# Kernel tuning notes

Measured on AMD Instinct MI355X. Metric: run time of the kernel, lower is better.

## Reference

```python
import jax, jax.numpy as jnp
import numpy as np

B, N, E, H = 2, 4096, 1024, 16
HD = E // H                      # head_dim = 64
R = 8                            # LoRA rank
LORA_SCALE = 16.0 / R            # alpha / r = 2.0
BUCKET_SIZES = (256, 64, 16)


def setup_inputs() -> dict:
    key = jax.random.key(0)
    ks = jax.random.split(key, 24)
    inp = {"x": jax.random.normal(ks[0], (B, N, E), jnp.float32)}
    inp["wb_coarse"] = jax.random.randint(ks[1], (B, N), 0, 16)
    inp["wb_mid"] = jax.random.randint(ks[2], (B, N), 0, 64)
    inp["wb_fine"] = jax.random.randint(ks[3], (B, N), 0, 256)
    i = 4
    for name in ("q", "k", "v", "o"):
        inp[f"W{name}"] = jax.random.normal(ks[i], (E, E), jnp.float32) / np.sqrt(E); i += 1
        inp[f"b{name}"] = jax.random.normal(ks[i], (E,), jnp.float32) * 0.01; i += 1
        inp[f"A{name}"] = jax.random.normal(ks[i], (R, E), jnp.float32) / np.sqrt(E); i += 1
        inp[f"B{name}"] = jax.random.normal(ks[i], (E, R), jnp.float32) * 0.01; i += 1
    return inp


def _lora(x, W, b, A, Bm):
    # F.linear(x, W, b) + scale * x @ A.T @ B.T   (dropout=0 in eval)
    return x @ W.T + b + LORA_SCALE * ((x @ A.T) @ Bm.T)


def _chunked_attn(q, k, v, bidx, C):
    # q,k,v: [BH, N, D]; bidx: [BH, N] int; C: chunk size (divides N)
    BH, Nn, D = q.shape
    sidx = jnp.argsort(bidx, axis=1)
    uidx = jnp.argsort(sidx, axis=1)
    g = lambda t, i: jnp.take_along_axis(t, i[..., None], axis=1)
    qs, ks_, vs = g(q, sidx), g(k, sidx), g(v, sidx)
    nc = Nn // C
    qs = qs.reshape(BH, nc, C, D)
    ks_ = ks_.reshape(BH, nc, C, D)
    vs = vs.reshape(BH, nc, C, D)
    # previous chunk (look-back of one chunk); chunk 0 has no previous -> masked
    k_prev = jnp.concatenate([jnp.zeros_like(ks_[:, :1]), ks_[:, :-1]], axis=1)
    v_prev = jnp.concatenate([jnp.zeros_like(vs[:, :1]), vs[:, :-1]], axis=1)
    k_cat = jnp.concatenate([k_prev, ks_], axis=2)   # [BH, nc, 2C, D]
    v_cat = jnp.concatenate([v_prev, vs], axis=2)
    scores = jnp.einsum('bncd,bnkd->bnck', qs, k_cat) / jnp.sqrt(jnp.asarray(D, qs.dtype))
    # mask look-back keys for chunk 0 (torch path attends only within chunk 0)
    chunk_ids = jnp.arange(nc)[:, None, None]        # [nc,1,1]
    key_pos = jnp.arange(2 * C)[None, None, :]       # [1,1,2C]
    neg = jnp.finfo(scores.dtype).min
    scores = jnp.where((chunk_ids == 0) & (key_pos < C), neg, scores)
    attn = jax.nn.softmax(scores, axis=-1)
    out = jnp.einsum('bnck,bnkd->bncd', attn, v_cat).reshape(BH, Nn, D)
    return jnp.take_along_axis(out, uidx[..., None], axis=1)


def reference(x, wb_coarse, wb_mid, wb_fine,
              Wq, bq, Aq, Bq, Wk, bk, Ak, Bk,
              Wv, bv, Av, Bv, Wo, bo, Ao, Bo):
    q = _lora(x, Wq, bq, Aq, Bq)
    k = _lora(x, Wk, bk, Ak, Bk)
    v = _lora(x, Wv, bv, Av, Bv)
    to_heads = lambda t: t.reshape(B, N, H, HD).transpose(0, 2, 1, 3).reshape(B * H, N, HD)
    qh, kh, vh = to_heads(q), to_heads(k), to_heads(v)
    expand = lambda w: jnp.broadcast_to(w[:, None, :], (B, H, N)).reshape(B * H, N)
    wbs = (expand(wb_coarse), expand(wb_mid), expand(wb_fine))
    outs = (_chunked_attn(qh, kh, vh, wbs[0], BUCKET_SIZES[0])
            + _chunked_attn(qh, kh, vh, wbs[1], BUCKET_SIZES[1])
            + _chunked_attn(qh, kh, vh, wbs[2], BUCKET_SIZES[2])) / 3.0
    outs = outs.reshape(B, H, N, HD).transpose(0, 2, 1, 3).reshape(B, N, E)
    return _lora(outs, Wo, bo, Ao, Bo)
```

## Files before the change

kernel.cpp:

```cpp
#include <hip/hip_runtime.h>
#include <cstdint>
#include <cstddef>

#define BDIM 2
#define NTOK 4096
#define EDIM 1024
#define HEADS 16
#define HDIM 64
#define MROWS (BDIM * NTOK)

typedef unsigned short u16;
typedef __attribute__((ext_vector_type(8))) short bf16x8;
typedef __attribute__((ext_vector_type(8))) unsigned short u16x8;
typedef __attribute__((ext_vector_type(4))) float f32x4;

#define MFMA(a, b, c) __builtin_amdgcn_mfma_f32_16x16x32_bf16(a, b, c, 0, 0, 0)
#define BAR() asm volatile("s_barrier" ::: "memory")
#define SETPRIO(p) __builtin_amdgcn_s_setprio(p)

__device__ inline void split2(float x, u16& h, u16& l) {
    union { float f; unsigned u; } a;
    a.f = x;
    unsigned uh = a.u + 0x7fff + ((a.u >> 16) & 1);
    h = (u16)(uh >> 16);
    union { unsigned u; float f; } hf; hf.u = (unsigned)h << 16;
    a.f = x - hf.f;
    unsigned ul = a.u + 0x7fff + ((a.u >> 16) & 1);
    l = (u16)(ul >> 16);
}

__device__ inline u16 bf16rne(float x) {
    union { float f; unsigned u; } a; a.f = x;
    unsigned r = a.u + 0x7fff + ((a.u >> 16) & 1);
    return (u16)(r >> 16);
}

#define GLL(gp, lp) __builtin_amdgcn_global_load_lds( \
    (const __attribute__((address_space(1))) unsigned*)(gp), \
    (__attribute__((address_space(3))) unsigned*)(lp), 16, 0, 0)

__global__ __launch_bounds__(256) void build_weff4_kernel(
    const float* __restrict__ W0, const float* __restrict__ A0, const float* __restrict__ B0,
    const float* __restrict__ W1, const float* __restrict__ A1, const float* __restrict__ B1,
    const float* __restrict__ W2, const float* __restrict__ A2, const float* __restrict__ B2,
    const float* __restrict__ W3, const float* __restrict__ A3, const float* __restrict__ B3,
    u16* __restrict__ dh0, u16* __restrict__ dl0,
    u16* __restrict__ dh1, u16* __restrict__ dl1,
    u16* __restrict__ dh2, u16* __restrict__ dl2,
    u16* __restrict__ dh3, u16* __restrict__ dl3)
{
    int s = blockIdx.y;
    const float* W = (s == 0) ? W0 : (s == 1) ? W1 : (s == 2) ? W2 : W3;
    const float* A = (s == 0) ? A0 : (s == 1) ? A1 : (s == 2) ? A2 : A3;
    const float* Bm = (s == 0) ? B0 : (s == 1) ? B1 : (s == 2) ? B2 : B3;
    u16* dh = (s == 0) ? dh0 : (s == 1) ? dh1 : (s == 2) ? dh2 : dh3;
    u16* dl = (s == 0) ? dl0 : (s == 1) ? dl1 : (s == 2) ? dl2 : dl3;

    int idx = blockIdx.x * 256 + threadIdx.x;
    int o = idx >> 10, i = idx & 1023;
    float sum = 0.f;
#pragma unroll
    for (int r = 0; r < 8; ++r) sum += Bm[o * 8 + r] * A[r * 1024 + i];
    float w = W[idx] + 2.0f * sum;
    u16 h, l;
    split2(w, h, l);
    dh[idx] = h; dl[idx] = l;
}

__global__ __launch_bounds__(256) void split_kernel(
    const float* __restrict__ src, u16* __restrict__ dh, u16* __restrict__ dl)
{
    int idx = blockIdx.x * 256 + threadIdx.x;
    float4 v = ((const float4*)src)[idx];
    ushort4 h, l;
    split2(v.x, h.x, l.x);
    split2(v.y, h.y, l.y);
    split2(v.z, h.z, l.z);
    split2(v.w, h.w, l.w);
    ((ushort4*)dh)[idx] = h;
    ((ushort4*)dl)[idx] = l;
}

__global__ __launch_bounds__(256) void sort3_kernel(
    const int* __restrict__ w0, const int* __restrict__ w1,
    const int* __restrict__ w2, int* __restrict__ sidx)
{
    __shared__ int sb[NTOK];
    __shared__ int cnt[32][256];
    __shared__ int gb[256];
    const int* srcs[3] = {w0, w1, w2};
    int t = threadIdx.x;
    const int* w = srcs[blockIdx.y] + blockIdx.x * NTOK;
    int* outp = sidx + ((int)blockIdx.y * BDIM + (int)blockIdx.x) * NTOK;

    for (int i = t; i < NTOK; i += 256) sb[i] = w[i];
    for (int i = t; i < 32 * 256; i += 256) ((int*)cnt)[i] = 0;
    __syncthreads();

    int g = t >> 3;
#pragma unroll
    for (int e = 0; e < 16; ++e)
        atomicAdd(&cnt[g][sb[g * 128 + (t & 7) + 8 * e]], 1);
    __syncthreads();

    int run = 0;
#pragma unroll
    for (int gg = 0; gg < 32; ++gg) {
        int c = cnt[gg][t];
        cnt[gg][t] = run;
        run += c;
    }
    gb[t] = run;
    __syncthreads();
    if (t == 0) {
        int acc = 0;
        for (int v = 0; v < 256; ++v) { int c = gb[v]; gb[v] = acc; acc += c; }
    }
    __syncthreads();
    for (int i = t; i < 32 * 256; i += 256) {
        int v = i & 255, gg = i >> 8;
        cnt[gg][v] += gb[v];
    }
    __syncthreads();

    if (t < 32) {
        int base = t * 128;
        for (int e = 0; e < 128; ++e) {
            int v = sb[base + e];
            int p = cnt[t][v]++;
            outp[p] = base + e;
        }
    }
}

__global__ __launch_bounds__(512, 2) void gemm_qk_kernel(
    const u16* __restrict__ Xh, const u16* __restrict__ Xl,
    const u16* __restrict__ Wh, const u16* __restrict__ Wl,
    const float* __restrict__ bq, const float* __restrict__ bk,
    u16* __restrict__ qh, u16* __restrict__ ql,
    u16* __restrict__ kh, u16* __restrict__ kl)
{
    __shared__ __align__(16) unsigned char smem[147456];
    u16* lds = (u16*)smem;
    const int PA_h = 0, PA_l = 8192, PB_h = 16384, PB_l = 20480;

    int t = threadIdx.x;
    int lane = t & 63, wave = t >> 6;
    int bid = blockIdx.x;
    int wg = (bid & 7) * 64 + (bid >> 3);
    int bx = wg & 15, by = wg >> 4;
    int m0 = by * 256, n0 = bx * 128;

    int lrow = lane & 15, lq = lane >> 4;
    size_t aoff = (size_t)(m0 + wave * 32 + lrow) * EDIM + lq * 8;
    size_t boff = (size_t)(n0 + wave * 16 + lrow) * EDIM + lq * 8;
    int slabA = wave * 2;
    int sA0 = (wave >> 1) * 4;
    int sB0 = (wave & 1) * 4;
    f32x4 acc[4][4] = {};

#pragma unroll
    for (int tt = 0; tt < 2; ++tt) {
        u16* sbuf = lds + tt * 24576;
        int kk = tt * 32;
        GLL(Xh + aoff + kk,             sbuf + PA_h + (slabA + 0) * 512);
        GLL(Xh + aoff + kk + 16 * EDIM, sbuf + PA_h + (slabA + 1) * 512);
        GLL(Xl + aoff + kk,             sbuf + PA_l + (slabA + 0) * 512);
        GLL(Xl + aoff + kk + 16 * EDIM, sbuf + PA_l + (slabA + 1) * 512);
        GLL(Wh + boff + kk, sbuf + PB_h + wave * 512);
        GLL(Wl + boff + kk, sbuf + PB_l + wave * 512);
    }
    asm volatile("s_waitcnt vmcnt(6)" ::: "memory");
    BAR();

    for (int t32 = 0; t32 < 32; ++t32) {
        u16* rb = lds + (t32 % 3) * 24576;
        u16* sbuf = lds + ((t32 + 2) % 3) * 24576;
        bool pf = (t32 + 2) < 32;
        int kn = (t32 + 2) * 32;
        bf16x8 bhf[4], blf[4];
#pragma unroll
        for (int p = 0; p < 4; ++p) {
            if (p == 0) {
#pragma unroll
                for (int j = 0; j < 4; ++j) {
                    bhf[j] = *(const bf16x8*)(rb + PB_h + (sB0 + j) * 512 + lane * 8);
                    blf[j] = *(const bf16x8*)(rb + PB_l + (sB0 + j) * 512 + lane * 8);
                }
            }
            bf16x8 aph = *(const bf16x8*)(rb + PA_h + (sA0 + p) * 512 + lane * 8);
            bf16x8 apl = *(const bf16x8*)(rb + PA_l + (sA0 + p) * 512 + lane * 8);
            if (pf) {
                if (p == 0) {
                    GLL(Xh + aoff + kn,             sbuf + PA_h + (slabA + 0) * 512);
                    GLL(Xh + aoff + kn + 16 * EDIM, sbuf + PA_h + (slabA + 1) * 512);
                } else if (p == 1) {
                    GLL(Xl + aoff + kn,             sbuf + PA_l + (slabA + 0) * 512);
                    GLL(Xl + aoff + kn + 16 * EDIM, sbuf + PA_l + (slabA + 1) * 512);
                } else if (p == 2) {
                    GLL(Wh + boff + kn, sbuf + PB_h + wave * 512);
                    GLL(Wl + boff + kn, sbuf + PB_l + wave * 512);
                }
            }
            BAR();
            SETPRIO(1);
#pragma unroll
            for (int j = 0; j < 4; ++j) {
                acc[p][j] = MFMA(aph, bhf[j], acc[p][j]);
                acc[p][j] = MFMA(aph, blf[j], acc[p][j]);
                acc[p][j] = MFMA(apl, bhf[j], acc[p][j]);
            }
            SETPRIO(0);
            if (p == 3) {
                if (pf) asm volatile("s_waitcnt vmcnt(6)" ::: "memory");
                else    asm volatile("s_waitcnt vmcnt(0)" ::: "memory");
            }
            BAR();
        }
    }

    int proj = n0 >> 10;
    const float* bias = proj ? bk : bq;
    u16* ohp = proj ? kh : qh;
    u16* olp = proj ? kl : ql;
    int wm = (wave >> 1) * 64, wn = (wave & 1) * 64;
    int q4 = lane >> 4, l16 = lane & 15;
    int cb = (n0 & 1023) + wn;
    float bj[4];
#pragma unroll
    for (int j = 0; j < 4; ++j) bj[j] = bias[cb + j * 16 + l16];
    float* repw = (float*)smem + wave * 2176;
    int r8 = lane >> 3, c8 = lane & 7;
#pragma unroll
    for (int gph = 0; gph < 2; ++gph) {
#pragma unroll
        for (int ii = 0; ii < 2; ++ii)
#pragma unroll
            for (int j = 0; j < 4; ++j)
#pragma unroll
                for (int r = 0; r < 4; ++r)
                    repw[(ii * 16 + q4 * 4 + r) * 68 + j * 16 + l16] =
                        acc[gph * 2 + ii][j][r] + bj[j];
#pragma unroll
        for (int rg = 0; rg < 4; ++rg) {
            int lr = rg * 8 + r8;
            float4 f0 = *(float4*)(repw + lr * 68 + c8 * 8);
            float4 f1 = *(float4*)(repw + lr * 68 + c8 * 8 + 4);
            float fa[8] = {f0.x, f0.y, f0.z, f0.w, f1.x, f1.y, f1.z, f1.w};
            size_t off = (size_t)(m0 + wm + gph * 32 + lr) * EDIM + cb + c8 * 8;
            u16x8 hv, lv;
#pragma unroll
            for (int e = 0; e < 8; ++e) {
                float v = fa[e];
                if (proj == 0) v *= 0.125f;
                u16 hh, ll;
                split2(v, hh, ll);
                hv[e] = hh; lv[e] = ll;
            }
            *(u16x8*)(ohp + off) = hv;
            *(u16x8*)(olp + off) = lv;
        }
    }
}

__global__ __launch_bounds__(512, 2) void gemm_v_kernel(
    const u16* __restrict__ Xh, const u16* __restrict__ Wv,
    const float* __restrict__ bv, u16* __restrict__ vh)
{
    __shared__ __align__(16) unsigned char smem[73728];
    u16* lds = (u16*)smem;

    int t = threadIdx.x;
    int lane = t & 63, wave = t >> 6;
    int bid = blockIdx.x;
    int wg = (bid & 7) * 32 + (bid >> 3);
    int bx = wg & 7, by = wg >> 3;
    int m0 = by * 256, nc0 = bx * 128;

    int lrow = lane & 15, lq = lane >> 4;
    size_t aoff = (size_t)(m0 + wave * 32 + lrow) * EDIM + lq * 8;
    size_t boff = (size_t)(nc0 + wave * 16 + lrow) * EDIM + lq * 8;
    int slabA = wave * 2;
    int sA0 = (wave >> 1) * 4;
    int sB0 = (wave & 1) * 4;
    f32x4 acc[4][4] = {};

#pragma unroll
    for (int tt = 0; tt < 2; ++tt) {
        u16* sbuf = lds + tt * 12288;
        int kk = tt * 32;
        GLL(Xh + aoff + kk,             sbuf + (slabA + 0) * 512);
        GLL(Xh + aoff + kk + 16 * EDIM, sbuf + (slabA + 1) * 512);
        GLL(Wv + boff + kk,             sbuf + 8192 + wave * 512);
    }
    asm volatile("s_waitcnt vmcnt(3)" ::: "memory");
    BAR();

    for (int t32 = 0; t32 < 32; ++t32) {
        u16* rb = lds + (t32 % 3) * 12288;
        u16* sbuf = lds + ((t32 + 2) % 3) * 12288;
        bool pf = (t32 + 2) < 32;
        int kn = (t32 + 2) * 32;

        bf16x8 bhf[4];
#pragma unroll
        for (int j = 0; j < 4; ++j)
            bhf[j] = *(const bf16x8*)(rb + 8192 + (sB0 + j) * 512 + lane * 8);
        bf16x8 a0 = *(const bf16x8*)(rb + (sA0 + 0) * 512 + lane * 8);
        bf16x8 a1 = *(const bf16x8*)(rb + (sA0 + 1) * 512 + lane * 8);
        if (pf) {
            GLL(Xh + aoff + kn,             sbuf + (slabA + 0) * 512);
            GLL(Xh + aoff + kn + 16 * EDIM, sbuf + (slabA + 1) * 512);
        }
        BAR();
        SETPRIO(1);
#pragma unroll
        for (int j = 0; j < 4; ++j) {
            acc[0][j] = MFMA(a0, bhf[j], acc[0][j]);
            acc[1][j] = MFMA(a1, bhf[j], acc[1][j]);
        }
        SETPRIO(0);
        BAR();

        bf16x8 a2 = *(const bf16x8*)(rb + (sA0 + 2) * 512 + lane * 8);
        bf16x8 a3 = *(const bf16x8*)(rb + (sA0 + 3) * 512 + lane * 8);
        if (pf) GLL(Wv + boff + kn, sbuf + 8192 + wave * 512);
        BAR();
        SETPRIO(1);
#pragma unroll
        for (int j = 0; j < 4; ++j) {
            acc[2][j] = MFMA(a2, bhf[j], acc[2][j]);
            acc[3][j] = MFMA(a3, bhf[j], acc[3][j]);
        }
        SETPRIO(0);
        if (pf) asm volatile("s_waitcnt vmcnt(3)" ::: "memory");
        else    asm volatile("s_waitcnt vmcnt(0)" ::: "memory");
        BAR();
    }

    int wm = (wave >> 1) * 64, wn = (wave & 1) * 64;
    int q4 = lane >> 4, l16 = lane & 15;
    int cb = nc0 + wn;
    float bj[4];
#pragma unroll
    for (int j = 0; j < 4; ++j) bj[j] = bv[cb + j * 16 + l16];
    float* repw = (float*)smem + wave * 2176;
    int r8 = lane >> 3, c8 = lane & 7;
#pragma unroll
    for (int gph = 0; gph < 2; ++gph) {
#pragma unroll
        for (int ii = 0; ii < 2; ++ii)
#pragma unroll
            for (int j = 0; j < 4; ++j)
#pragma unroll
                for (int r = 0; r < 4; ++r)
                    repw[(ii * 16 + q4 * 4 + r) * 68 + j * 16 + l16] =
                        acc[gph * 2 + ii][j][r] + bj[j];
#pragma unroll
        for (int rg = 0; rg < 4; ++rg) {
            int lr = rg * 8 + r8;
            float4 f0 = *(float4*)(repw + lr * 68 + c8 * 8);
            float4 f1 = *(float4*)(repw + lr * 68 + c8 * 8 + 4);
            float fa[8] = {f0.x, f0.y, f0.z, f0.w, f1.x, f1.y, f1.z, f1.w};
            size_t off = (size_t)(m0 + wm + gph * 32 + lr) * EDIM + cb + c8 * 8;
            u16x8 hv;
#pragma unroll
            for (int e = 0; e < 8; ++e) hv[e] = bf16rne(fa[e]);
            *(u16x8*)(vh + off) = hv;
        }
    }
}

__global__ __launch_bounds__(512, 2) void gemm_o_kernel(
    const u16* __restrict__ Xh, const u16* __restrict__ Xl,
    const u16* __restrict__ Wh, const u16* __restrict__ Wl,
    const float* __restrict__ bias, float* __restrict__ Y)
{
    __shared__ __align__(16) unsigned char smem[147456];
    u16* lds = (u16*)smem;
    const int PA_h = 0, PA_l = 8192, PB_h = 16384, PB_l = 20480;

    int t = threadIdx.x;
    int lane = t & 63, wave = t >> 6;
    int bid = blockIdx.x;
    int wg = (bid & 7) * 32 + (bid >> 3);
    int bx = wg & 7, by = wg >> 3;
    int m0 = by * 256, n0 = bx * 128;

    int lrow = lane & 15, lq = lane >> 4;
    size_t aoff = (size_t)(m0 + wave * 32 + lrow) * EDIM + lq * 8;
    size_t boff = (size_t)(n0 + wave * 16 + lrow) * EDIM + lq * 8;
    int slabA = wave * 2;
    int sA0 = (wave >> 1) * 4;
    int sB0 = (wave & 1) * 4;
    f32x4 acc[4][4] = {};

#pragma unroll
    for (int tt = 0; tt < 2; ++tt) {
        u16* sbuf = lds + tt * 24576;
        int kk = tt * 32;
        GLL(Xh + aoff + kk,             sbuf + PA_h + (slabA + 0) * 512);
        GLL(Xh + aoff + kk + 16 * EDIM, sbuf + PA_h + (slabA + 1) * 512);
        GLL(Xl + aoff + kk,             sbuf + PA_l + (slabA + 0) * 512);
        GLL(Xl + aoff + kk + 16 * EDIM, sbuf + PA_l + (slabA + 1) * 512);
        GLL(Wh + boff + kk, sbuf + PB_h + wave * 512);
        GLL(Wl + boff + kk, sbuf + PB_l + wave * 512);
    }
    asm volatile("s_waitcnt vmcnt(6)" ::: "memory");
    BAR();

    for (int t32 = 0; t32 < 32; ++t32) {
        u16* rb = lds + (t32 % 3) * 24576;
        u16* sbuf = lds + ((t32 + 2) % 3) * 24576;
        bool pf = (t32 + 2) < 32;
        int kn = (t32 + 2) * 32;
        bf16x8 bhf[4], blf[4];
#pragma unroll
        for (int p = 0; p < 4; ++p) {
            if (p == 0) {
#pragma unroll
                for (int j = 0; j < 4; ++j) {
                    bhf[j] = *(const bf16x8*)(rb + PB_h + (sB0 + j) * 512 + lane * 8);
                    blf[j] = *(const bf16x8*)(rb + PB_l + (sB0 + j) * 512 + lane * 8);
                }
            }
            bf16x8 aph = *(const bf16x8*)(rb + PA_h + (sA0 + p) * 512 + lane * 8);
            bf16x8 apl = *(const bf16x8*)(rb + PA_l + (sA0 + p) * 512 + lane * 8);
            if (pf) {
                if (p == 0) {
                    GLL(Xh + aoff + kn,             sbuf + PA_h + (slabA + 0) * 512);
                    GLL(Xh + aoff + kn + 16 * EDIM, sbuf + PA_h + (slabA + 1) * 512);
                } else if (p == 1) {
                    GLL(Xl + aoff + kn,             sbuf + PA_l + (slabA + 0) * 512);
                    GLL(Xl + aoff + kn + 16 * EDIM, sbuf + PA_l + (slabA + 1) * 512);
                } else if (p == 2) {
                    GLL(Wh + boff + kn, sbuf + PB_h + wave * 512);
                    GLL(Wl + boff + kn, sbuf + PB_l + wave * 512);
                }
            }
            BAR();
            SETPRIO(1);
#pragma unroll
            for (int j = 0; j < 4; ++j) {
                acc[p][j] = MFMA(aph, bhf[j], acc[p][j]);
                acc[p][j] = MFMA(aph, blf[j], acc[p][j]);
                acc[p][j] = MFMA(apl, bhf[j], acc[p][j]);
            }
            SETPRIO(0);
            if (p == 3) {
                if (pf) asm volatile("s_waitcnt vmcnt(6)" ::: "memory");
                else    asm volatile("s_waitcnt vmcnt(0)" ::: "memory");
            }
            BAR();
        }
    }

    int wm = (wave >> 1) * 64, wn = (wave & 1) * 64;
    int col_in = lane & 15, rquad = lane >> 4;
#pragma unroll
    for (int j = 0; j < 4; ++j) {
        int col = n0 + wn + j * 16 + col_in;
        float bvv = bias[col];
#pragma unroll
        for (int i = 0; i < 4; ++i) {
            int mbase = m0 + wm + i * 16 + rquad * 4;
#pragma unroll
            for (int r = 0; r < 4; ++r)
                Y[(size_t)(mbase + r) * EDIM + col] = acc[i][j][r] + bvv;
        }
    }
}

template <int C, bool ACC, bool OSPLIT>
__global__ __launch_bounds__(256, 3) void attn_mfma_kernel(
    const u16* __restrict__ Qh, const u16* __restrict__ Ql,
    const u16* __restrict__ Kh, const u16* __restrict__ Kl,
    const u16* __restrict__ Vh, const int* __restrict__ sidx,
    float* __restrict__ out, u16* __restrict__ osh, u16* __restrict__ osl)
{
    __shared__ u16 KfH[2][4096], KfL[2][4096];
    __shared__ u16 VL[64 * 72];
    __shared__ u16 PbH[4 * 16 * 56];

    int t = threadIdx.x;
    int lane = t & 63, wave = t >> 6;
    int quad = lane >> 4, l16 = lane & 15;
    int bh = blockIdx.y, b = bh >> 4, h = bh & 15;
    int p0 = blockIdx.x * 128;
    const int* sxb = sidx + b * NTOK;

    int ptile[2], ws_[2], we_[2];
    bf16x8 qhf[2][2], qlf[2][2];
#pragma unroll
    for (int tq = 0; tq < 2; ++tq) {
        ptile[tq] = p0 + wave * 32 + tq * 16;
        int c = ptile[tq] / C;
        ws_[tq] = (c > 0) ? (c - 1) * C : 0;
        we_[tq] = (c + 1) * C;
        int qrow = sxb[ptile[tq] + l16];
        size_t rb = (size_t)(b * NTOK + qrow) * EDIM + h * HDIM + quad * 8;
#pragma unroll
        for (int kk = 0; kk < 2; ++kk) {
            qhf[tq][kk] = *(const bf16x8*)(Qh + rb + kk * 32);
            qlf[tq][kk] = *(const bf16x8*)(Ql + rb + kk * 32);
        }
    }

    f32x4 oacc[2][4] = {};
    float lpart[2][4] = {};
    float mrun[2] = {-1e30f, -1e30f};

    int c0 = p0 / C, c1 = (p0 + 127) / C;
    int kmin = (c0 > 0) ? (c0 - 1) * C : 0;
    int kmax = (c1 + 1) * C;
    int nsteps = (kmax - kmin + 63) >> 6;

    {
        int tok = sxb[min(kmin + wave * 16 + l16, NTOK - 1)];
        size_t rb = (size_t)(b * NTOK + tok) * EDIM + h * HDIM + quad * 8;
        GLL(Kh + rb,      &KfH[0][(wave * 2 + 0) * 512]);
        GLL(Kh + rb + 32, &KfH[0][(wave * 2 + 1) * 512]);
        GLL(Kl + rb,      &KfL[0][(wave * 2 + 0) * 512]);
        GLL(Kl + rb + 32, &KfL[0][(wave * 2 + 1) * 512]);
        bf16x8 vreg[2];
#pragma unroll
        for (int it = 0; it < 2; ++it) {
            int c = it * 256 + t;
            int key = c & 63, dg = c >> 6;
            int tok2 = sxb[min(kmin + key, NTOK - 1)];
            vreg[it] = *(const bf16x8*)(Vh + (size_t)(b * NTOK + tok2) * EDIM + h * HDIM + dg * 8);
        }
#pragma unroll
        for (int it = 0; it < 2; ++it) {
            int c = it * 256 + t;
            int key = c & 63, dg = c >> 6;
#pragma unroll
            for (int e = 0; e < 8; ++e)
                VL[(dg * 8 + e) * 72 + key] = (u16)vreg[it][e];
        }
        asm volatile("s_waitcnt vmcnt(0)" ::: "memory");
        __syncthreads();
    }

    int pb = 0;
    for (int s = 0; s < nsteps; ++s) {
        int ks = kmin + s * 64;
        int nk = min(64, kmax - ks);
        bool pf = (s + 1) < nsteps;
        bf16x8 vreg[2];
        if (pf) {
            int ks2 = ks + 64;
            int tok = sxb[min(ks2 + wave * 16 + l16, NTOK - 1)];
            size_t rb = (size_t)(b * NTOK + tok) * EDIM + h * HDIM + quad * 8;
            GLL(Kh + rb,      &KfH[pb ^ 1][(wave * 2 + 0) * 512]);
            GLL(Kh + rb + 32, &KfH[pb ^ 1][(wave * 2 + 1) * 512]);
            GLL(Kl + rb,      &KfL[pb ^ 1][(wave * 2 + 0) * 512]);
            GLL(Kl + rb + 32, &KfL[pb ^ 1][(wave * 2 + 1) * 512]);
#pragma unroll
            for (int it = 0; it < 2; ++it) {
                int c = it * 256 + t;
                int key = c & 63, dg = c >> 6;
                int tok2 = sxb[min(ks2 + key, NTOK - 1)];
                vreg[it] = *(const bf16x8*)(Vh + (size_t)(b * NTOK + tok2) * EDIM + h * HDIM + dg * 8);
            }
        }

        int jlo0 = max(ks, ws_[0]) - ks, jhi0 = min(ks + nk, we_[0]) - ks;
        int jlo1 = max(ks, ws_[1]) - ks, jhi1 = min(ks + nk, we_[1]) - ks;
        bool e0 = jlo0 < jhi0, e1 = jlo1 < jhi1;
        if (e0 || e1) {
            int glo = e0 ? (e1 ? min(jlo0, jlo1) : jlo0) : jlo1;
            int ghi = e0 ? (e1 ? max(jhi0, jhi1) : jhi0) : jhi1;
            const u16* kfh = &KfH[pb][0];
            const u16* kfl = &KfL[pb][0];

            for (int g0 = glo & ~31; g0 < ghi; g0 += 32) {
                int s0i = g0 >> 4;
                int s1i = min(s0i + 1, 3);
                bf16x8 kh0[2], kl0[2], kh1[2], kl1[2];
#pragma unroll
                for (int kk = 0; kk < 2; ++kk) {
                    kh0[kk] = *(const bf16x8*)(kfh + ((s0i * 2 + kk) * 64 + lane) * 8);
                    kl0[kk] = *(const bf16x8*)(kfl + ((s0i * 2 + kk) * 64 + lane) * 8);
                    kh1[kk] = *(const bf16x8*)(kfh + ((s1i * 2 + kk) * 64 + lane) * 8);
                    kl1[kk] = *(const bf16x8*)(kfl + ((s1i * 2 + kk) * 64 + lane) * 8);
                }
#pragma unroll
                for (int tq = 0; tq < 2; ++tq) {
                    int jl = tq ? jlo1 : jlo0, jh = tq ? jhi1 : jhi0;
                    bool v0 = (g0 >= jl) && (g0 < jh);
                    bool v1 = (g0 + 16 >= jl) && (g0 + 16 < jh);
                    if (!v0 && !v1) continue;
                    f32x4 sa = {0.f, 0.f, 0.f, 0.f}, sb2 = {0.f, 0.f, 0.f, 0.f};
                    if (v0) {
                        sa = MFMA(qhf[tq][0], kh0[0], sa);
                        sa = MFMA(qhf[tq][0], kl0[0], sa);
                        sa = MFMA(qlf[tq][0], kh0[0], sa);
                        sa = MFMA(qhf[tq][1], kh0[1], sa);
                        sa = MFMA(qhf[tq][1], kl0[1], sa);
                        sa = MFMA(qlf[tq][1], kh0[1], sa);
                    }
                    if (v1) {
                        sb2 = MFMA(qhf[tq][0], kh1[0], sb2);
                        sb2 = MFMA(qhf[tq][0], kl1[0], sb2);
                        sb2 = MFMA(qlf[tq][0], kh1[0], sb2);
                        sb2 = MFMA(qhf[tq][1], kh1[1], sb2);
                        sb2 = MFMA(qhf[tq][1], kl1[1], sb2);
                        sb2 = MFMA(qlf[tq][1], kh1[1], sb2);
                    }
                    float smax = -1e30f;
                    if (v0) smax = fmaxf(smax, fmaxf(fmaxf(sa[0], sa[1]), fmaxf(sa[2], sa[3])));
                    if (v1) smax = fmaxf(smax, fmaxf(fmaxf(sb2[0], sb2[1]), fmaxf(sb2[2], sb2[3])));
                    smax = fmaxf(smax, __shfl_xor(smax, 1));
                    smax = fmaxf(smax, __shfl_xor(smax, 2));
                    smax = fmaxf(smax, __shfl_xor(smax, 4));
                    smax = fmaxf(smax, __shfl_xor(smax, 8));
                    float mold = mrun[tq];
                    float mnew = mold;
                    if (smax > mold + 8.0f) {
                        mnew = smax;
                        mrun[tq] = mnew;
                        float alpha = __expf(mold - mnew);
#pragma unroll
                        for (int r = 0; r < 4; ++r) lpart[tq][r] *= alpha;
#pragma unroll
                        for (int dt = 0; dt < 4; ++dt) {
                            oacc[tq][dt][0] *= alpha; oacc[tq][dt][1] *= alpha;
                            oacc[tq][dt][2] *= alpha; oacc[tq][dt][3] *= alpha;
                        }
                    }
                    u16* pbh = PbH + wave * 896;
#pragma unroll
                    for (int r = 0; r < 4; ++r) {
                        float pa = v0 ? __expf(sa[r] - mnew) : 0.f;
                        float pbv = v1 ? __expf(sb2[r] - mnew) : 0.f;
                        lpart[tq][r] += pa + pbv;
                        pbh[(quad * 4 + r) * 56 + l16] = bf16rne(pa);
                        pbh[(quad * 4 + r) * 56 + 16 + l16] = bf16rne(pbv);
                    }
                    bf16x8 ph = *(const bf16x8*)(pbh + l16 * 56 + quad * 8);
                    int kh2 = g0 >> 5;
#pragma unroll
                    for (int dt = 0; dt < 4; ++dt) {
                        bf16x8 vv = *(const bf16x8*)(VL + (dt * 16 + l16) * 72 + kh2 * 32 + quad * 8);
                        oacc[tq][dt] = MFMA(ph, vv, oacc[tq][dt]);
                    }
                }
            }
        }

        asm volatile("s_waitcnt vmcnt(0)" ::: "memory");
        __syncthreads();
        if (pf) {
#pragma unroll
            for (int it = 0; it < 2; ++it) {
                int c = it * 256 + t;
                int key = c & 63, dg = c >> 6;
#pragma unroll
                for (int e = 0; e < 8; ++e)
                    VL[(dg * 8 + e) * 72 + key] = (u16)vreg[it][e];
            }
        }
        __syncthreads();
        pb ^= 1;
    }

#pragma unroll
    for (int tq = 0; tq < 2; ++tq) {
        float inv[4];
#pragma unroll
        for (int r = 0; r < 4; ++r) {
            float v = lpart[tq][r];
            v += __shfl_xor(v, 1);
            v += __shfl_xor(v, 2);
            v += __shfl_xor(v, 4);
            v += __shfl_xor(v, 8);
            inv[r] = 1.0f / (3.0f * v);
        }
#pragma unroll
        for (int r = 0; r < 4; ++r) {
            int tok = sxb[ptile[tq] + quad * 4 + r];
            size_t base = (size_t)(b * NTOK + tok) * EDIM + h * HDIM + l16;
            if (OSPLIT) {
#pragma unroll
                for (int dt = 0; dt < 4; ++dt) {
                    float v = out[base + dt * 16] + oacc[tq][dt][r] * inv[r];
                    u16 hh, ll;
                    split2(v, hh, ll);
                    osh[base + dt * 16] = hh;
                    osl[base + dt * 16] = ll;
                }
            } else if (ACC) {
#pragma unroll
                for (int dt = 0; dt < 4; ++dt)
                    out[base + dt * 16] += oacc[tq][dt][r] * inv[r];
            } else {
#pragma unroll
                for (int dt = 0; dt < 4; ++dt)
                    out[base + dt * 16] = oacc[tq][dt][r] * inv[r];
            }
        }
    }
}

extern "C" void kernel_launch(void* const* d_in, const int* in_sizes, int n_in,
                              void* d_out, int out_size, void* d_ws, size_t ws_size,
                              hipStream_t stream)
{
    const float* x   = (const float*)d_in[0];
    const int*   wbc = (const int*)d_in[1];
    const int*   wbm = (const int*)d_in[2];
    const int*   wbf = (const int*)d_in[3];
    const float* Wq = (const float*)d_in[4],  *bq = (const float*)d_in[5];
    const float* Aq = (const float*)d_in[6],  *Bq = (const float*)d_in[7];
    const float* Wk = (const float*)d_in[8],  *bk = (const float*)d_in[9];
    const float* Ak = (const float*)d_in[10], *Bk = (const float*)d_in[11];
    const float* Wv = (const float*)d_in[12], *bv = (const float*)d_in[13];
    const float* Av = (const float*)d_in[14], *Bv = (const float*)d_in[15];
    const float* Wo = (const float*)d_in[16], *bo = (const float*)d_in[17];
    const float* Ao = (const float*)d_in[18], *Bo = (const float*)d_in[19];

    const size_t EE  = (size_t)EDIM * EDIM;
    const size_t BNE = (size_t)MROWS * EDIM;

    char* wsb = (char*)d_ws;
    float* ab = (float*)wsb;                        wsb += BNE * 4;
    u16* xh = (u16*)wsb;                            wsb += BNE * 2;
    u16* xl = (u16*)wsb;                            wsb += BNE * 2;
    u16* qh = (u16*)wsb;                            wsb += BNE * 2;
    u16* ql = (u16*)wsb;                            wsb += BNE * 2;
    u16* kh = (u16*)wsb;                            wsb += BNE * 2;
    u16* kl = (u16*)wsb;                            wsb += BNE * 2;
    u16* vh = (u16*)wsb;                            wsb += BNE * 2;
    u16* wh_all = (u16*)wsb;                        wsb += 3 * EE * 2;
    u16* wl_all = (u16*)wsb;                        wsb += 3 * EE * 2;
    u16* woh = (u16*)wsb;                           wsb += EE * 2;
    u16* wol = (u16*)wsb;                           wsb += EE * 2;
    int* sidx = (int*)wsb;                          wsb += 3 * BDIM * NTOK * 4;

    split_kernel<<<BNE / 1024, 256, 0, stream>>>(x, xh, xl);

    build_weff4_kernel<<<dim3(4096, 4), 256, 0, stream>>>(
        Wq, Aq, Bq, Wk, Ak, Bk, Wv, Av, Bv, Wo, Ao, Bo,
        wh_all + 0 * EE, wl_all + 0 * EE,
        wh_all + 1 * EE, wl_all + 1 * EE,
        wh_all + 2 * EE, wl_all + 2 * EE,
        woh, wol);

    sort3_kernel<<<dim3(BDIM, 3), 256, 0, stream>>>(wbc, wbm, wbf, sidx);

    gemm_qk_kernel<<<512, 512, 0, stream>>>(xh, xl, wh_all, wl_all,
                                            bq, bk, qh, ql, kh, kl);
    gemm_v_kernel<<<256, 512, 0, stream>>>(xh, wh_all + 2 * EE, bv, vh);

    dim3 ga(NTOK / 128, BDIM * HEADS);
    attn_mfma_kernel<256, false, false><<<ga, 256, 0, stream>>>(
        qh, ql, kh, kl, vh, sidx + 0 * BDIM * NTOK, ab, xh, xl);
    attn_mfma_kernel<64, true, false><<<ga, 256, 0, stream>>>(
        qh, ql, kh, kl, vh, sidx + 1 * BDIM * NTOK, ab, xh, xl);
    attn_mfma_kernel<16, true, true><<<ga, 256, 0, stream>>>(
        qh, ql, kh, kl, vh, sidx + 2 * BDIM * NTOK, ab, xh, xl);

    gemm_o_kernel<<<256, 512, 0, stream>>>(xh, xl, woh, wol, bo, (float*)d_out);
}
```

Before: 510.0 us.

## Load K fragments directly from global, double-buffer V in LDS with one barrier

```diff
diff --git a/kernel.cpp b/kernel.cpp
--- a/kernel.cpp
+++ b/kernel.cpp
@@ -478,8 +478,7 @@
     const u16* __restrict__ Vh, const int* __restrict__ sidx,
     float* __restrict__ out, u16* __restrict__ osh, u16* __restrict__ osl)
 {
-    __shared__ u16 KfH[2][4096], KfL[2][4096];
-    __shared__ u16 VL[64 * 72];
+    __shared__ u16 VL[2][64 * 72];
     __shared__ u16 PbH[4 * 16 * 56];
 
     int t = threadIdx.x;
@@ -487,7 +486,9 @@
     int quad = lane >> 4, l16 = lane & 15;
     int bh = blockIdx.y, b = bh >> 4, h = bh & 15;
     int p0 = blockIdx.x * 128;
+    const size_t bbase = (size_t)b * NTOK;
     const int* sxb = sidx + b * NTOK;
+    const int hoff = h * HDIM;
 
     int ptile[2], ws_[2], we_[2];
     bf16x8 qhf[2][2], qlf[2][2];
@@ -498,7 +499,7 @@
         ws_[tq] = (c > 0) ? (c - 1) * C : 0;
         we_[tq] = (c + 1) * C;
         int qrow = sxb[ptile[tq] + l16];
-        size_t rb = (size_t)(b * NTOK + qrow) * EDIM + h * HDIM + quad * 8;
+        size_t rb = (bbase + qrow) * EDIM + hoff + quad * 8;
 #pragma unroll
         for (int kk = 0; kk < 2; ++kk) {
             qhf[tq][kk] = *(const bf16x8*)(Qh + rb + kk * 32);
@@ -515,54 +516,33 @@
     int kmax = (c1 + 1) * C;
     int nsteps = (kmax - kmin + 63) >> 6;
 
+    int vkey = t & 63, vdg = t >> 6;
+    int vkey2 = vkey, vdg2 = vdg + 4;
+
+    bf16x8 vreg0, vreg1;
     {
-        int tok = sxb[min(kmin + wave * 16 + l16, NTOK - 1)];
-        size_t rb = (size_t)(b * NTOK + tok) * EDIM + h * HDIM + quad * 8;
-        GLL(Kh + rb,      &KfH[0][(wave * 2 + 0) * 512]);
-        GLL(Kh + rb + 32, &KfH[0][(wave * 2 + 1) * 512]);
-        GLL(Kl + rb,      &KfL[0][(wave * 2 + 0) * 512]);
-        GLL(Kl + rb + 32, &KfL[0][(wave * 2 + 1) * 512]);
-        bf16x8 vreg[2];
-#pragma unroll
-        for (int it = 0; it < 2; ++it) {
-            int c = it * 256 + t;
-            int key = c & 63, dg = c >> 6;
-            int tok2 = sxb[min(kmin + key, NTOK - 1)];
-            vreg[it] = *(const bf16x8*)(Vh + (size_t)(b * NTOK + tok2) * EDIM + h * HDIM + dg * 8);
-        }
-#pragma unroll
-        for (int it = 0; it < 2; ++it) {
-            int c = it * 256 + t;
-            int key = c & 63, dg = c >> 6;
-#pragma unroll
-            for (int e = 0; e < 8; ++e)
-                VL[(dg * 8 + e) * 72 + key] = (u16)vreg[it][e];
-        }
-        asm volatile("s_waitcnt vmcnt(0)" ::: "memory");
-        __syncthreads();
-    }
-
-    int pb = 0;
+        int tk0 = sxb[min(kmin + vkey, NTOK - 1)];
+        vreg0 = *(const bf16x8*)(Vh + (bbase + tk0) * EDIM + hoff + vdg * 8);
+        vreg1 = *(const bf16x8*)(Vh + (bbase + tk0) * EDIM + hoff + vdg2 * 8);
+    }
+
     for (int s = 0; s < nsteps; ++s) {
         int ks = kmin + s * 64;
         int nk = min(64, kmax - ks);
         bool pf = (s + 1) < nsteps;
-        bf16x8 vreg[2];
+        u16* vl = &VL[s & 1][0];
+
+#pragma unroll
+        for (int e = 0; e < 8; ++e) {
+            vl[(vdg * 8 + e) * 72 + vkey] = (u16)vreg0[e];
+            vl[(vdg2 * 8 + e) * 72 + vkey2] = (u16)vreg1[e];
+        }
+        __syncthreads();
+
         if (pf) {
-            int ks2 = ks + 64;
-            int tok = sxb[min(ks2 + wave * 16 + l16, NTOK - 1)];
-            size_t rb = (size_t)(b * NTOK + tok) * EDIM + h * HDIM + quad * 8;
-            GLL(Kh + rb,      &KfH[pb ^ 1][(wave * 2 + 0) * 512]);
-            GLL(Kh + rb + 32, &KfH[pb ^ 1][(wave * 2 + 1) * 512]);
-            GLL(Kl + rb,      &KfL[pb ^ 1][(wave * 2 + 0) * 512]);
-            GLL(Kl + rb + 32, &KfL[pb ^ 1][(wave * 2 + 1) * 512]);
-#pragma unroll
-            for (int it = 0; it < 2; ++it) {
-                int c = it * 256 + t;
-                int key = c & 63, dg = c >> 6;
-                int tok2 = sxb[min(ks2 + key, NTOK - 1)];
-                vreg[it] = *(const bf16x8*)(Vh + (size_t)(b * NTOK + tok2) * EDIM + h * HDIM + dg * 8);
-            }
+            int tk0 = sxb[min(ks + 64 + vkey, NTOK - 1)];
+            vreg0 = *(const bf16x8*)(Vh + (bbase + tk0) * EDIM + hoff + vdg * 8);
+            vreg1 = *(const bf16x8*)(Vh + (bbase + tk0) * EDIM + hoff + vdg2 * 8);
         }
 
         int jlo0 = max(ks, ws_[0]) - ks, jhi0 = min(ks + nk, we_[0]) - ks;
@@ -571,19 +551,21 @@
         if (e0 || e1) {
             int glo = e0 ? (e1 ? min(jlo0, jlo1) : jlo0) : jlo1;
             int ghi = e0 ? (e1 ? max(jhi0, jhi1) : jhi0) : jhi1;
-            const u16* kfh = &KfH[pb][0];
-            const u16* kfl = &KfL[pb][0];
 
             for (int g0 = glo & ~31; g0 < ghi; g0 += 32) {
                 int s0i = g0 >> 4;
                 int s1i = min(s0i + 1, 3);
+                int tok0 = sxb[min(ks + s0i * 16 + l16, NTOK - 1)];
+                int tok1 = sxb[min(ks + s1i * 16 + l16, NTOK - 1)];
+                size_t ra0 = (bbase + tok0) * EDIM + hoff + quad * 8;
+                size_t ra1 = (bbase + tok1) * EDIM + hoff + quad * 8;
                 bf16x8 kh0[2], kl0[2], kh1[2], kl1[2];
 #pragma unroll
                 for (int kk = 0; kk < 2; ++kk) {
-                    kh0[kk] = *(const bf16x8*)(kfh + ((s0i * 2 + kk) * 64 + lane) * 8);
-                    kl0[kk] = *(const bf16x8*)(kfl + ((s0i * 2 + kk) * 64 + lane) * 8);
-                    kh1[kk] = *(const bf16x8*)(kfh + ((s1i * 2 + kk) * 64 + lane) * 8);
-                    kl1[kk] = *(const bf16x8*)(kfl + ((s1i * 2 + kk) * 64 + lane) * 8);
+                    kh0[kk] = *(const bf16x8*)(Kh + ra0 + kk * 32);
+                    kl0[kk] = *(const bf16x8*)(Kl + ra0 + kk * 32);
+                    kh1[kk] = *(const bf16x8*)(Kh + ra1 + kk * 32);
+                    kl1[kk] = *(const bf16x8*)(Kl + ra1 + kk * 32);
                 }
 #pragma unroll
                 for (int tq = 0; tq < 2; ++tq) {
@@ -592,6 +574,7 @@
                     bool v1 = (g0 + 16 >= jl) && (g0 + 16 < jh);
                     if (!v0 && !v1) continue;
                     f32x4 sa = {0.f, 0.f, 0.f, 0.f}, sb2 = {0.f, 0.f, 0.f, 0.f};
+                    SETPRIO(1);
                     if (v0) {
                         sa = MFMA(qhf[tq][0], kh0[0], sa);
                         sa = MFMA(qhf[tq][0], kl0[0], sa);
@@ -608,6 +591,7 @@
                         sb2 = MFMA(qhf[tq][1], kl1[1], sb2);
                         sb2 = MFMA(qlf[tq][1], kh1[1], sb2);
                     }
+                    SETPRIO(0);
                     float smax = -1e30f;
                     if (v0) smax = fmaxf(smax, fmaxf(fmaxf(sa[0], sa[1]), fmaxf(sa[2], sa[3])));
                     if (v1) smax = fmaxf(smax, fmaxf(fmaxf(sb2[0], sb2[1]), fmaxf(sb2[2], sb2[3])));
@@ -640,29 +624,16 @@
                     }
                     bf16x8 ph = *(const bf16x8*)(pbh + l16 * 56 + quad * 8);
                     int kh2 = g0 >> 5;
+                    SETPRIO(1);
 #pragma unroll
                     for (int dt = 0; dt < 4; ++dt) {
-                        bf16x8 vv = *(const bf16x8*)(VL + (dt * 16 + l16) * 72 + kh2 * 32 + quad * 8);
+                        bf16x8 vv = *(const bf16x8*)(vl + (dt * 16 + l16) * 72 + kh2 * 32 + quad * 8);
                         oacc[tq][dt] = MFMA(ph, vv, oacc[tq][dt]);
                     }
+                    SETPRIO(0);
                 }
             }
         }
-
-        asm volatile("s_waitcnt vmcnt(0)" ::: "memory");
-        __syncthreads();
-        if (pf) {
-#pragma unroll
-            for (int it = 0; it < 2; ++it) {
-                int c = it * 256 + t;
-                int key = c & 63, dg = c >> 6;
-#pragma unroll
-                for (int e = 0; e < 8; ++e)
-                    VL[(dg * 8 + e) * 72 + key] = (u16)vreg[it][e];
-            }
-        }
-        __syncthreads();
-        pb ^= 1;
     }
 
 #pragma unroll
@@ -680,7 +651,7 @@
 #pragma unroll
         for (int r = 0; r < 4; ++r) {
             int tok = sxb[ptile[tq] + quad * 4 + r];
-            size_t base = (size_t)(b * NTOK + tok) * EDIM + h * HDIM + l16;
+            size_t base = (bbase + tok) * EDIM + hoff + l16;
             if (OSPLIT) {
 #pragma unroll
                 for (int dt = 0; dt < 4; ++dt) {
```

Result: slower. 554.5 us (+8.7%).
